# Optimization experiments

Measured on AMD Instinct MI355X. Metric: run time of the kernel, lower is better.

The kernel has to match this reference:

```python
import jax, jax.numpy as jnp
import numpy as np

NEG = -1000000000.0

def setup_inputs() -> dict:
    key = jax.random.key(0)
    k1, k2, k3, k4 = jax.random.split(key, 4)
    B, T, D, V = 64, 512, 768, 20
    embeddings = jax.random.normal(k1, (B, T, D), dtype=jnp.float32)
    embeddings_mask = jax.random.randint(k2, (B, T), 0, 2, dtype=jnp.int32)
    value_mask = jax.random.randint(k3, (B, V), 0, 2, dtype=jnp.int32)
    value_weight = jax.random.normal(k4, (V, D), dtype=jnp.float32)
    return {"embeddings": embeddings, "embeddings_mask": embeddings_mask,
            "value_mask": value_mask, "value_weight": value_weight}

def reference(embeddings, embeddings_mask, value_mask, value_weight):
    # value attention: scores[b,t,v] = <emb[b,t], W[v]>  (torch does bcast-mul-sum)
    emb_mask = embeddings_mask.astype(jnp.float32)          # (B,T)
    scores = jnp.einsum('btd,vd->btv', embeddings, value_weight)
    scores = scores * emb_mask[:, :, None]                   # mask tokens
    value_scores = scores.sum(axis=1)                        # (B,V)
    value_scores = value_scores + (1.0 - value_mask.astype(jnp.float32)) * NEG
    value_probs = jax.nn.softmax(value_scores, axis=-1)      # (B,V)
    value_embedding = jnp.einsum('bv,vd->bd', value_probs, value_weight)
    # attention pooling over tokens using value_embedding as query
    pooling_scores = jnp.einsum('btd,bd->bt', embeddings, value_embedding)
    pooling_scores = pooling_scores + (1.0 - emb_mask) * NEG
    pooling_probs = jax.nn.softmax(pooling_scores, axis=-1)  # (B,T)
    pooled_embedding = jnp.einsum('btd,bt->bd', embeddings, pooling_probs)
    return (value_embedding, pooled_embedding, value_probs, pooling_probs)
```

## Files before the change

kernel.cpp:

```cpp
#include <hip/hip_runtime.h>
#include <math.h>

#define B 64
#define T 512
#define D 768
#define V 20
#define NEG -1000000000.0f
#define TCH 32
#define NCH (T / TCH)

__global__ __launch_bounds__(256) void k_masked_sum(
    const float* __restrict__ emb, const int* __restrict__ emask,
    float* __restrict__ part) {
  int b = blockIdx.x / NCH;
  int c = blockIdx.x % NCH;
  int tid = threadIdx.x;
  __shared__ int sm[TCH];
  if (tid < TCH) sm[tid] = emask[b * T + c * TCH + tid];
  __syncthreads();
  float a0 = 0.f, a1 = 0.f, a2 = 0.f;
  const float* eb = emb + (size_t)b * T * D + (size_t)c * TCH * D;
  for (int tt = 0; tt < TCH; ++tt) {
    if (sm[tt]) {
      const float* e = eb + (size_t)tt * D + tid;
      a0 += e[0];
      a1 += e[256];
      a2 += e[512];
    }
  }
  float* p = part + (size_t)blockIdx.x * D + tid;
  p[0] = a0;
  p[256] = a1;
  p[512] = a2;
}

__global__ __launch_bounds__(256) void k_value(
    const float* __restrict__ part, const int* __restrict__ vmask,
    const float* __restrict__ W, float* __restrict__ out_vemb,
    float* __restrict__ out_vprobs) {
  int b = blockIdx.x;
  int tid = threadIdx.x;
  __shared__ float msum[D];
  __shared__ float sc[V];
  __shared__ float pr[V];
  for (int k = 0; k < 3; ++k) {
    int d = tid + 256 * k;
    float s = 0.f;
    for (int c = 0; c < NCH; ++c) s += part[((size_t)(b * NCH + c)) * D + d];
    msum[d] = s;
  }
  __syncthreads();
  int wave = tid >> 6, lane = tid & 63;
  for (int v = wave; v < V; v += 4) {
    float p = 0.f;
    for (int j = 0; j < 12; ++j) {
      int d = lane + 64 * j;
      p += msum[d] * W[(size_t)v * D + d];
    }
    for (int off = 32; off; off >>= 1) p += __shfl_down(p, off, 64);
    if (lane == 0) sc[v] = p + (vmask[b * V + v] ? 0.f : NEG);
  }
  __syncthreads();
  if (tid == 0) {
    float m = sc[0];
    for (int v = 1; v < V; ++v) m = fmaxf(m, sc[v]);
    float s = 0.f;
    for (int v = 0; v < V; ++v) {
      float e = expf(sc[v] - m);
      pr[v] = e;
      s += e;
    }
    float inv = 1.f / s;
    for (int v = 0; v < V; ++v) {
      pr[v] *= inv;
      out_vprobs[b * V + v] = pr[v];
    }
  }
  __syncthreads();
  for (int k = 0; k < 3; ++k) {
    int d = tid + 256 * k;
    float a = 0.f;
    for (int v = 0; v < V; ++v) a += pr[v] * W[(size_t)v * D + d];
    out_vemb[(size_t)b * D + d] = a;
  }
}

__global__ __launch_bounds__(256) void k_pool_scores(
    const float* __restrict__ emb, const int* __restrict__ emask,
    const float* __restrict__ vemb, float* __restrict__ scores) {
  int wave = threadIdx.x >> 6, lane = threadIdx.x & 63;
  int w = blockIdx.x * 4 + wave;
  int b = w >> 9;
  int t = w & 511;
  if (emask[b * T + t] == 0) {
    if (lane == 0) scores[b * T + t] = NEG;
    return;
  }
  const float* e = emb + ((size_t)b * T + t) * D;
  const float* ve = vemb + (size_t)b * D;
  float p = 0.f;
  for (int j = 0; j < 12; ++j) {
    int d = lane + 64 * j;
    p += e[d] * ve[d];
  }
  for (int off = 32; off; off >>= 1) p += __shfl_down(p, off, 64);
  if (lane == 0) scores[b * T + t] = p;
}

__global__ __launch_bounds__(256) void k_softmax_T(
    const float* __restrict__ scores, float* __restrict__ probs) {
  int b = blockIdx.x, tid = threadIdx.x;
  int wave = tid >> 6, lane = tid & 63;
  float s0 = scores[b * T + tid];
  float s1 = scores[b * T + 256 + tid];
  float m = fmaxf(s0, s1);
  __shared__ float redm[4];
  __shared__ float reds[4];
  for (int off = 32; off; off >>= 1) m = fmaxf(m, __shfl_down(m, off, 64));
  if (lane == 0) redm[wave] = m;
  __syncthreads();
  m = fmaxf(fmaxf(redm[0], redm[1]), fmaxf(redm[2], redm[3]));
  float e0 = expf(s0 - m), e1 = expf(s1 - m);
  float s = e0 + e1;
  for (int off = 32; off; off >>= 1) s += __shfl_down(s, off, 64);
  if (lane == 0) reds[wave] = s;
  __syncthreads();
  s = reds[0] + reds[1] + reds[2] + reds[3];
  float inv = 1.f / s;
  probs[b * T + tid] = e0 * inv;
  probs[b * T + 256 + tid] = e1 * inv;
}

__global__ __launch_bounds__(256) void k_pool_partial(
    const float* __restrict__ emb, const float* __restrict__ probs,
    float* __restrict__ part) {
  int b = blockIdx.x / NCH;
  int c = blockIdx.x % NCH;
  int tid = threadIdx.x;
  __shared__ float wts[TCH];
  if (tid < TCH) wts[tid] = probs[b * T + c * TCH + tid];
  __syncthreads();
  float a0 = 0.f, a1 = 0.f, a2 = 0.f;
  const float* eb = emb + (size_t)b * T * D + (size_t)c * TCH * D;
  for (int tt = 0; tt < TCH; ++tt) {
    float wv = wts[tt];
    if (wv != 0.f) {
      const float* e = eb + (size_t)tt * D + tid;
      a0 += wv * e[0];
      a1 += wv * e[256];
      a2 += wv * e[512];
    }
  }
  float* p = part + (size_t)blockIdx.x * D + tid;
  p[0] = a0;
  p[256] = a1;
  p[512] = a2;
}

__global__ __launch_bounds__(256) void k_reduce_part(
    const float* __restrict__ part, float* __restrict__ pooled) {
  int b = blockIdx.x, tid = threadIdx.x;
  for (int k = 0; k < 3; ++k) {
    int d = tid + 256 * k;
    float s = 0.f;
    for (int c = 0; c < NCH; ++c) s += part[((size_t)(b * NCH + c)) * D + d];
    pooled[(size_t)b * D + d] = s;
  }
}

extern "C" void kernel_launch(void* const* d_in, const int* in_sizes, int n_in,
                              void* d_out, int out_size, void* d_ws,
                              size_t ws_size, hipStream_t stream) {
  const float* emb = (const float*)d_in[0];
  const int* emask = (const int*)d_in[1];
  const int* vmask = (const int*)d_in[2];
  const float* W = (const float*)d_in[3];

  float* out = (float*)d_out;
  float* vemb_out = out;
  float* pooled_out = out + B * D;
  float* vprobs_out = out + 2 * B * D;
  float* pprobs_out = out + 2 * B * D + B * V;

  float* ws = (float*)d_ws;
  float* part = ws;
  float* scores = ws + B * NCH * D;

  k_masked_sum<<<B * NCH, 256, 0, stream>>>(emb, emask, part);
  k_value<<<B, 256, 0, stream>>>(part, vmask, W, vemb_out, vprobs_out);
  k_pool_scores<<<B * T / 4, 256, 0, stream>>>(emb, emask, vemb_out, scores);
  k_softmax_T<<<B, 256, 0, stream>>>(scores, pprobs_out);
  k_pool_partial<<<B * NCH, 256, 0, stream>>>(emb, pprobs_out, part);
  k_reduce_part<<<B, 256, 0, stream>>>(part, pooled_out);
}
```

Measured before the change: 183.4 us.

## Fuse pooling scores, softmax and weighted sum with online softmax; vectorize loads

```diff
diff --git a/kernel.cpp b/kernel.cpp
--- a/kernel.cpp
+++ b/kernel.cpp
@@ -4,34 +4,30 @@
 #define B 64
 #define T 512
 #define D 768
+#define D4 (D / 4)
 #define V 20
 #define NEG -1000000000.0f
 #define TCH 32
 #define NCH (T / TCH)
 
-__global__ __launch_bounds__(256) void k_masked_sum(
-    const float* __restrict__ emb, const int* __restrict__ emask,
-    float* __restrict__ part) {
+__global__ __launch_bounds__(192) void k_masked_sum(
+    const float4* __restrict__ emb4, const int* __restrict__ emask,
+    float4* __restrict__ part4) {
   int b = blockIdx.x / NCH;
   int c = blockIdx.x % NCH;
   int tid = threadIdx.x;
   __shared__ int sm[TCH];
   if (tid < TCH) sm[tid] = emask[b * T + c * TCH + tid];
   __syncthreads();
-  float a0 = 0.f, a1 = 0.f, a2 = 0.f;
-  const float* eb = emb + (size_t)b * T * D + (size_t)c * TCH * D;
+  float4 a = {0.f, 0.f, 0.f, 0.f};
+  const float4* eb = emb4 + ((size_t)b * T + (size_t)c * TCH) * D4 + tid;
   for (int tt = 0; tt < TCH; ++tt) {
     if (sm[tt]) {
-      const float* e = eb + (size_t)tt * D + tid;
-      a0 += e[0];
-      a1 += e[256];
-      a2 += e[512];
-    }
-  }
-  float* p = part + (size_t)blockIdx.x * D + tid;
-  p[0] = a0;
-  p[256] = a1;
-  p[512] = a2;
+      float4 e = eb[(size_t)tt * D4];
+      a.x += e.x; a.y += e.y; a.z += e.z; a.w += e.w;
+    }
+  }
+  part4[(size_t)blockIdx.x * D4 + tid] = a;
 }
 
 __global__ __launch_bounds__(256) void k_value(
@@ -85,86 +81,117 @@
   }
 }
 
-__global__ __launch_bounds__(256) void k_pool_scores(
-    const float* __restrict__ emb, const int* __restrict__ emask,
-    const float* __restrict__ vemb, float* __restrict__ scores) {
-  int wave = threadIdx.x >> 6, lane = threadIdx.x & 63;
-  int w = blockIdx.x * 4 + wave;
-  int b = w >> 9;
-  int t = w & 511;
-  if (emask[b * T + t] == 0) {
-    if (lane == 0) scores[b * T + t] = NEG;
-    return;
-  }
-  const float* e = emb + ((size_t)b * T + t) * D;
-  const float* ve = vemb + (size_t)b * D;
-  float p = 0.f;
-  for (int j = 0; j < 12; ++j) {
-    int d = lane + 64 * j;
-    p += e[d] * ve[d];
-  }
-  for (int off = 32; off; off >>= 1) p += __shfl_down(p, off, 64);
-  if (lane == 0) scores[b * T + t] = p;
-}
-
-__global__ __launch_bounds__(256) void k_softmax_T(
-    const float* __restrict__ scores, float* __restrict__ probs) {
-  int b = blockIdx.x, tid = threadIdx.x;
-  int wave = tid >> 6, lane = tid & 63;
-  float s0 = scores[b * T + tid];
-  float s1 = scores[b * T + 256 + tid];
-  float m = fmaxf(s0, s1);
-  __shared__ float redm[4];
-  __shared__ float reds[4];
-  for (int off = 32; off; off >>= 1) m = fmaxf(m, __shfl_down(m, off, 64));
-  if (lane == 0) redm[wave] = m;
-  __syncthreads();
-  m = fmaxf(fmaxf(redm[0], redm[1]), fmaxf(redm[2], redm[3]));
-  float e0 = expf(s0 - m), e1 = expf(s1 - m);
-  float s = e0 + e1;
-  for (int off = 32; off; off >>= 1) s += __shfl_down(s, off, 64);
-  if (lane == 0) reds[wave] = s;
-  __syncthreads();
-  s = reds[0] + reds[1] + reds[2] + reds[3];
-  float inv = 1.f / s;
-  probs[b * T + tid] = e0 * inv;
-  probs[b * T + 256 + tid] = e1 * inv;
-}
-
-__global__ __launch_bounds__(256) void k_pool_partial(
-    const float* __restrict__ emb, const float* __restrict__ probs,
-    float* __restrict__ part) {
+__global__ __launch_bounds__(256) void k_fused_pool(
+    const float4* __restrict__ emb4, const int* __restrict__ emask,
+    const float4* __restrict__ vemb4, float* __restrict__ scores,
+    float* __restrict__ pm, float* __restrict__ pl,
+    float4* __restrict__ pacc4) {
   int b = blockIdx.x / NCH;
   int c = blockIdx.x % NCH;
   int tid = threadIdx.x;
-  __shared__ float wts[TCH];
-  if (tid < TCH) wts[tid] = probs[b * T + c * TCH + tid];
-  __syncthreads();
-  float a0 = 0.f, a1 = 0.f, a2 = 0.f;
-  const float* eb = emb + (size_t)b * T * D + (size_t)c * TCH * D;
-  for (int tt = 0; tt < TCH; ++tt) {
-    float wv = wts[tt];
-    if (wv != 0.f) {
-      const float* e = eb + (size_t)tt * D + tid;
-      a0 += wv * e[0];
-      a1 += wv * e[256];
-      a2 += wv * e[512];
-    }
-  }
-  float* p = part + (size_t)blockIdx.x * D + tid;
-  p[0] = a0;
-  p[256] = a1;
-  p[512] = a2;
-}
-
-__global__ __launch_bounds__(256) void k_reduce_part(
-    const float* __restrict__ part, float* __restrict__ pooled) {
+  int wave = tid >> 6, lane = tid & 63;
+  __shared__ int sm[TCH];
+  __shared__ float lm[4], ll[4];
+  __shared__ float lacc[4][D];
+  if (tid < TCH) sm[tid] = emask[b * T + c * TCH + tid];
+  __syncthreads();
+
+  float4 ve[3];
+  for (int j = 0; j < 3; ++j) ve[j] = vemb4[(size_t)b * D4 + lane + 64 * j];
+
+  float m = NEG, l = 0.f;
+  float4 acc[3];
+  for (int j = 0; j < 3; ++j) acc[j] = {0.f, 0.f, 0.f, 0.f};
+
+  const float4* eb = emb4 + ((size_t)b * T + (size_t)c * TCH) * D4;
+  for (int tt = wave; tt < TCH; tt += 4) {
+    if (!sm[tt]) {
+      if (lane == 0) scores[b * T + c * TCH + tt] = NEG;
+      continue;
+    }
+    float4 e[3];
+    for (int j = 0; j < 3; ++j) e[j] = eb[(size_t)tt * D4 + lane + 64 * j];
+    float p = 0.f;
+    for (int j = 0; j < 3; ++j)
+      p += e[j].x * ve[j].x + e[j].y * ve[j].y + e[j].z * ve[j].z +
+           e[j].w * ve[j].w;
+    for (int off = 32; off; off >>= 1) p += __shfl_xor(p, off, 64);
+    if (lane == 0) scores[b * T + c * TCH + tt] = p;
+    if (p > m) {
+      float scale = expf(m - p);
+      l *= scale;
+      for (int j = 0; j < 3; ++j) {
+        acc[j].x *= scale; acc[j].y *= scale;
+        acc[j].z *= scale; acc[j].w *= scale;
+      }
+      m = p;
+    }
+    float w = expf(p - m);
+    l += w;
+    for (int j = 0; j < 3; ++j) {
+      acc[j].x += w * e[j].x; acc[j].y += w * e[j].y;
+      acc[j].z += w * e[j].z; acc[j].w += w * e[j].w;
+    }
+  }
+
+  if (lane == 0) { lm[wave] = m; ll[wave] = l; }
+  for (int j = 0; j < 3; ++j)
+    *(float4*)&lacc[wave][4 * (lane + 64 * j)] = acc[j];
+  __syncthreads();
+
+  __shared__ float co[4];
+  __shared__ float sM, sL;
+  if (tid == 0) {
+    float M = fmaxf(fmaxf(lm[0], lm[1]), fmaxf(lm[2], lm[3]));
+    float L = 0.f;
+    for (int w2 = 0; w2 < 4; ++w2) {
+      co[w2] = expf(lm[w2] - M);
+      L += ll[w2] * co[w2];
+    }
+    sM = M; sL = L;
+    pm[blockIdx.x] = M;
+    pl[blockIdx.x] = L;
+  }
+  __syncthreads();
+  if (tid < D4) {
+    float4 s = {0.f, 0.f, 0.f, 0.f};
+    for (int w2 = 0; w2 < 4; ++w2) {
+      float cw = co[w2];
+      float4 a = *(float4*)&lacc[w2][4 * tid];
+      s.x += cw * a.x; s.y += cw * a.y; s.z += cw * a.z; s.w += cw * a.w;
+    }
+    pacc4[(size_t)blockIdx.x * D4 + tid] = s;
+  }
+}
+
+__global__ __launch_bounds__(256) void k_pool_final(
+    const float* __restrict__ pm, const float* __restrict__ pl,
+    const float* __restrict__ pacc, const float* __restrict__ scores,
+    const int* __restrict__ emask, float* __restrict__ pooled,
+    float* __restrict__ pprobs) {
   int b = blockIdx.x, tid = threadIdx.x;
+  __shared__ float co[NCH];
+  __shared__ float sM, sinvL;
+  if (tid == 0) {
+    float M = NEG;
+    for (int c = 0; c < NCH; ++c) M = fmaxf(M, pm[b * NCH + c]);
+    float L = 0.f;
+    for (int c = 0; c < NCH; ++c) L += pl[b * NCH + c] * expf(pm[b * NCH + c] - M);
+    float invL = 1.f / L;
+    for (int c = 0; c < NCH; ++c) co[c] = expf(pm[b * NCH + c] - M) * invL;
+    sM = M; sinvL = invL;
+  }
+  __syncthreads();
   for (int k = 0; k < 3; ++k) {
     int d = tid + 256 * k;
     float s = 0.f;
-    for (int c = 0; c < NCH; ++c) s += part[((size_t)(b * NCH + c)) * D + d];
+    for (int c = 0; c < NCH; ++c) s += pacc[((size_t)(b * NCH + c)) * D + d] * co[c];
     pooled[(size_t)b * D + d] = s;
+  }
+  for (int k = 0; k < 2; ++k) {
+    int t = tid + 256 * k;
+    pprobs[b * T + t] =
+        emask[b * T + t] ? expf(scores[b * T + t] - sM) * sinvL : 0.f;
   }
 }
 
@@ -185,11 +212,15 @@
   float* ws = (float*)d_ws;
   float* part = ws;
   float* scores = ws + B * NCH * D;
-
-  k_masked_sum<<<B * NCH, 256, 0, stream>>>(emb, emask, part);
+  float* pm = scores + B * T;
+  float* pl = pm + B * NCH;
+
+  k_masked_sum<<<B * NCH, 192, 0, stream>>>((const float4*)emb, emask,
+                                            (float4*)part);
   k_value<<<B, 256, 0, stream>>>(part, vmask, W, vemb_out, vprobs_out);
-  k_pool_scores<<<B * T / 4, 256, 0, stream>>>(emb, emask, vemb_out, scores);
-  k_softmax_T<<<B, 256, 0, stream>>>(scores, pprobs_out);
-  k_pool_partial<<<B * NCH, 256, 0, stream>>>(emb, pprobs_out, part);
-  k_reduce_part<<<B, 256, 0, stream>>>(part, pooled_out);
-}
+  k_fused_pool<<<B * NCH, 256, 0, stream>>>((const float4*)emb, emask,
+                                            (const float4*)vemb_out, scores, pm,
+                                            pl, (float4*)part);
+  k_pool_final<<<B, 256, 0, stream>>>(pm, pl, part, scores, emask, pooled_out,
+                                      pprobs_out);
+}
```

Result: faster. 171.7 us (-6.3%).
